# Performance work log

Measured on AMD Instinct MI355X. Metric: run time of the kernel, lower is better.

## Reference

```python
import jax, jax.numpy as jnp
import numpy as np

B, S, H, V, L = 2, 1024, 2048, 32000, 8


def _ternary(w):
    """BitNet-1.58 style per-tensor ternary quantization with STE."""
    scale = jnp.mean(jnp.abs(w))
    wq = jnp.clip(jnp.round(w / (scale + 1e-8)), -1.0, 1.0) * scale
    # straight-through: forward value is wq, gradient flows to w
    return w + jax.lax.stop_gradient(wq - w)


def _layernorm(x, g, b, eps=1e-5):
    m = jnp.mean(x, axis=-1, keepdims=True)
    v = jnp.var(x, axis=-1, keepdims=True)
    return (x - m) / jnp.sqrt(v + eps) * g + b


def setup_inputs() -> dict:
    key = jax.random.key(0)
    ks = jax.random.split(key, 5)
    return {
        "input_ids": jax.random.randint(ks[0], (B, S), 0, V),
        "embed": jax.random.normal(ks[1], (V, H), jnp.float32) * 0.02,
        "layer_w": jax.random.normal(ks[2], (L, H, H), jnp.float32) * 0.02,
        "layer_b": jnp.zeros((L, H), jnp.float32),
        "ln_g": jnp.ones((L, H), jnp.float32),
        "ln_b": jnp.zeros((L, H), jnp.float32),
        "final_g": jnp.ones((H,), jnp.float32),
        "final_b": jnp.zeros((H,), jnp.float32),
        "head_w": jax.random.normal(ks[3], (V, H), jnp.float32) * 0.02,
    }


def reference(input_ids, embed, layer_w, layer_b, ln_g, ln_b, final_g, final_b, head_w):
    # embedding lookup: (B, S, H)
    h = embed[input_ids]

    def step(h, params):
        w, b, g, bb = params
        y = jnp.einsum("bsh,oh->bso", h, _ternary(w)) + b  # ternary linear
        h = _layernorm(y + h, g, bb)                        # residual + LN
        return h, None

    h, _ = jax.lax.scan(step, h, (layer_w, layer_b, ln_g, ln_b))
    h = _layernorm(h, final_g, final_b)
    logits = jnp.einsum("bsh,vh->bsv", h, _ternary(head_w))  # (B, S, V)
    return logits
```

## Files before the change

kernel.cpp:

```cpp
#include <hip/hip_runtime.h>


#define H 2048
#define MTOK 2048
#define VOC 32000
#define NL 8
#define BK 64

typedef __attribute__((ext_vector_type(8))) _Float16 f16x8;
typedef __attribute__((ext_vector_type(4))) float f32x4;

__device__ __forceinline__ unsigned short f2h(float f) {
  _Float16 h = (_Float16)f;
  union { _Float16 h; unsigned short u; } v; v.h = h;
  return v.u;
}

__global__ void abssum_kernel(const float* __restrict__ w, int n, long nstride,
                              float* __restrict__ out) {
  __shared__ float sbuf[4];
  const float* wp = w + (long)blockIdx.y * nstride;
  int tid = blockIdx.x * blockDim.x + threadIdx.x;
  int stride = gridDim.x * blockDim.x * 4;
  float s = 0.f;
  for (int i = tid * 4; i < n; i += stride) {
    float4 v = *reinterpret_cast<const float4*>(wp + i);
    s += fabsf(v.x) + fabsf(v.y) + fabsf(v.z) + fabsf(v.w);
  }
#pragma unroll
  for (int off = 32; off > 0; off >>= 1) s += __shfl_down(s, off);
  if ((threadIdx.x & 63) == 0) sbuf[threadIdx.x >> 6] = s;
  __syncthreads();
  if (threadIdx.x == 0) atomicAdd(out + blockIdx.y, sbuf[0] + sbuf[1] + sbuf[2] + sbuf[3]);
}

__global__ void quantize_kernel(const float* __restrict__ w, int n,
                                const float* __restrict__ sumptr, float cnt,
                                unsigned short* __restrict__ T) {
  float scale = *sumptr / cnt;
  float spe = scale + 1e-8f;
  int tid = blockIdx.x * blockDim.x + threadIdx.x;
  int stride = gridDim.x * blockDim.x * 4;
  for (int i = tid * 4; i < n; i += stride) {
    float4 v = *reinterpret_cast<const float4*>(w + i);
    ushort4 t;
    t.x = f2h(fminf(fmaxf(rintf(v.x / spe), -1.f), 1.f));
    t.y = f2h(fminf(fmaxf(rintf(v.y / spe), -1.f), 1.f));
    t.z = f2h(fminf(fmaxf(rintf(v.z / spe), -1.f), 1.f));
    t.w = f2h(fminf(fmaxf(rintf(v.w / spe), -1.f), 1.f));
    *reinterpret_cast<ushort4*>(T + i) = t;
  }
}

__global__ void gather_split_kernel(const int* __restrict__ ids, const float* __restrict__ embed,
                                    float* __restrict__ h, unsigned short* __restrict__ act) {
  int t = blockIdx.x;
  long src = (long)ids[t] * H;
  long dst = (long)t * H;
  for (int c = threadIdx.x * 4; c < H; c += blockDim.x * 4) {
    float4 v = *reinterpret_cast<const float4*>(embed + src + c);
    *reinterpret_cast<float4*>(h + dst + c) = v;
    ushort4 u;
    u.x = f2h(v.x); u.y = f2h(v.y); u.z = f2h(v.z); u.w = f2h(v.w);
    *reinterpret_cast<ushort4*>(act + dst + c) = u;
  }
}

__device__ __forceinline__ float block_sum(float v, float* sbuf) {
#pragma unroll
  for (int off = 32; off > 0; off >>= 1) v += __shfl_down(v, off);
  int lane = threadIdx.x & 63, w = threadIdx.x >> 6;
  if (lane == 0) sbuf[w] = v;
  __syncthreads();
  float r = sbuf[0] + sbuf[1] + sbuf[2] + sbuf[3];
  __syncthreads();
  return r;
}

__global__ void ln_kernel(const float* __restrict__ x_in, const float* __restrict__ resid,
                          const float* __restrict__ g, const float* __restrict__ b,
                          float* __restrict__ hout, unsigned short* __restrict__ act) {
  __shared__ float sbuf[4];
  int t = blockIdx.x;
  long base = (long)t * H;
  int c0 = threadIdx.x * 8;
  float x[8];
#pragma unroll
  for (int j = 0; j < 8; j += 4) {
    float4 v = *reinterpret_cast<const float4*>(x_in + base + c0 + j);
    x[j] = v.x; x[j + 1] = v.y; x[j + 2] = v.z; x[j + 3] = v.w;
  }
  if (resid != nullptr) {
#pragma unroll
    for (int j = 0; j < 8; j += 4) {
      float4 v = *reinterpret_cast<const float4*>(resid + base + c0 + j);
      x[j] += v.x; x[j + 1] += v.y; x[j + 2] += v.z; x[j + 3] += v.w;
    }
  }
  float s = 0.f;
#pragma unroll
  for (int j = 0; j < 8; ++j) s += x[j];
  s = block_sum(s, sbuf);
  float m = s * (1.f / H);
  float vs = 0.f;
#pragma unroll
  for (int j = 0; j < 8; ++j) { float d = x[j] - m; vs += d * d; }
  vs = block_sum(vs, sbuf);
  float r = 1.f / sqrtf(vs * (1.f / H) + 1e-5f);
  float o[8];
#pragma unroll
  for (int j = 0; j < 8; ++j) o[j] = (x[j] - m) * r * g[c0 + j] + b[c0 + j];
  if (hout != nullptr) {
#pragma unroll
    for (int j = 0; j < 8; j += 4) {
      float4 v; v.x = o[j]; v.y = o[j + 1]; v.z = o[j + 2]; v.w = o[j + 3];
      *reinterpret_cast<float4*>(hout + base + c0 + j) = v;
    }
  }
#pragma unroll
  for (int j = 0; j < 8; j += 4) {
    ushort4 u;
    u.x = f2h(o[j]); u.y = f2h(o[j + 1]); u.z = f2h(o[j + 2]); u.w = f2h(o[j + 3]);
    *reinterpret_cast<ushort4*>(act + base + c0 + j) = u;
  }
}

__device__ __forceinline__ void gll16(const void* g, void* l) {
  __builtin_amdgcn_global_load_lds((const __attribute__((address_space(1))) void*)g,
                                   (__attribute__((address_space(3))) void*)l, 16, 0, 0);
}

template <int ROWS>
__device__ __forceinline__ void stage_tile(unsigned short* sdst, const unsigned short* G,
                                           long row0, int k0, long ldk, int tid) {
  int wv = tid >> 6, lane = tid & 63;
  int c = lane & 7;
  int r8 = lane >> 3;
  int cs = c ^ r8;
#pragma unroll
  for (int i = 0; i < ROWS / 32; ++i) {
    int blk = i * 4 + wv;
    int row = blk * 8 + r8;
    const unsigned short* g = G + (row0 + row) * ldk + (k0 + cs * 8);
    gll16((const void*)g, (void*)(sdst + blk * 512));
  }
}

template <int TBM, int TBN, int WR, int WC, int MF, int NF, bool HAS_BIAS>
__global__ __launch_bounds__(256)
void gemm_t(const unsigned short* __restrict__ A, const unsigned short* __restrict__ Bt,
            const float* __restrict__ bias, const float* __restrict__ sumptr, float cnt,
            float* __restrict__ C, int N, int K, int nrb) {
  __shared__ unsigned short sA[2][TBM * BK];
  __shared__ unsigned short sB[2][TBN * BK];
  int tid = threadIdx.x;
  int lane = tid & 63, wid = tid >> 6;
  int wr = wid / WC, wc = wid % WC;

  int nwg = gridDim.x;
  int bid = blockIdx.x;
  int chunk = nwg >> 3;
  int swz = (bid & 7) * chunk + (bid >> 3);
  int rb = swz % nrb, cbl = swz / nrb;
  long row0 = (long)rb * TBM;
  long col0 = (long)cbl * TBN;

  f32x4 acc[MF][NF] = {};

  int rsel = lane & 15;
  int hi = lane >> 4;
  int lx = lane & 7;

  int NT = K >> 6;
  stage_tile<TBM>(sA[0], A, row0, 0, K, tid);
  stage_tile<TBN>(sB[0], Bt, col0, 0, K, tid);

  for (int t = 0; t < NT; ++t) {
    __syncthreads();
    int nb = (t + 1) & 1;
    if (t + 1 < NT) {
      stage_tile<TBM>(sA[nb], A, row0, (t + 1) << 6, K, tid);
      stage_tile<TBN>(sB[nb], Bt, col0, (t + 1) << 6, K, tid);
    }
    const unsigned short* pA = sA[t & 1];
    const unsigned short* pB = sB[t & 1];
#pragma unroll
    for (int kk = 0; kk < 2; ++kk) {
      int seg = (kk * 4 + hi) ^ lx;
      f16x8 af[MF], bf[NF];
#pragma unroll
      for (int f = 0; f < MF; ++f) {
        int ra = wr * (MF * 16) + f * 16 + rsel;
        af[f] = *reinterpret_cast<const f16x8*>(&pA[ra * BK + seg * 8]);
      }
#pragma unroll
      for (int f = 0; f < NF; ++f) {
        int rn = wc * (NF * 16) + f * 16 + rsel;
        bf[f] = *reinterpret_cast<const f16x8*>(&pB[rn * BK + seg * 8]);
      }
#pragma unroll
      for (int mf = 0; mf < MF; ++mf)
#pragma unroll
        for (int nf = 0; nf < NF; ++nf)
          acc[mf][nf] = __builtin_amdgcn_mfma_f32_16x16x32_f16(af[mf], bf[nf], acc[mf][nf], 0, 0, 0);
    }
  }

  float scale = *sumptr / cnt;
#pragma unroll
  for (int mf = 0; mf < MF; ++mf) {
    long grow0 = row0 + wr * (MF * 16) + mf * 16 + hi * 4;
#pragma unroll
    for (int nf = 0; nf < NF; ++nf) {
      long gcol = col0 + wc * (NF * 16) + nf * 16 + rsel;
      float bv = HAS_BIAS ? bias[gcol] : 0.f;
#pragma unroll
      for (int r = 0; r < 4; ++r) {
        C[(grow0 + r) * (long)N + gcol] = acc[mf][nf][r] * scale + bv;
      }
    }
  }
}

extern "C" void kernel_launch(void* const* d_in, const int* in_sizes, int n_in,
                              void* d_out, int out_size, void* d_ws, size_t ws_size,
                              hipStream_t stream) {
  const int* input_ids = (const int*)d_in[0];
  const float* embed   = (const float*)d_in[1];
  const float* layer_w = (const float*)d_in[2];
  const float* layer_b = (const float*)d_in[3];
  const float* ln_g    = (const float*)d_in[4];
  const float* ln_b    = (const float*)d_in[5];
  const float* final_g = (const float*)d_in[6];
  const float* final_b = (const float*)d_in[7];
  const float* head_w  = (const float*)d_in[8];
  float* out = (float*)d_out;

  char* ws = (char*)d_ws;
  size_t off = 0;
  auto take = [&](size_t bytes) -> void* {
    void* p = ws + off;
    off = (off + bytes + 255) & ~(size_t)255;
    return p;
  };
  float* sums        = (float*)take(16 * sizeof(float));
  unsigned short* Tl = (unsigned short*)take((size_t)H * H * 2);
  unsigned short* Th = (unsigned short*)take((size_t)VOC * H * 2);
  float* hbuf        = (float*)take((size_t)MTOK * H * 4);
  float* ybuf        = (float*)take((size_t)MTOK * H * 4);
  unsigned short* act = (unsigned short*)take((size_t)MTOK * H * 2);
  (void)ws_size; (void)in_sizes; (void)n_in; (void)out_size;

  hipMemsetAsync(sums, 0, 16 * sizeof(float), stream);

  abssum_kernel<<<dim3(512, NL), 256, 0, stream>>>(layer_w, H * H, (long)H * H, sums);
  abssum_kernel<<<dim3(2048, 1), 256, 0, stream>>>(head_w, VOC * H, 0, sums + 8);

  quantize_kernel<<<4096, 256, 0, stream>>>(head_w, VOC * H, sums + 8, (float)((size_t)VOC * H), Th);

  gather_split_kernel<<<MTOK, 256, 0, stream>>>(input_ids, embed, hbuf, act);

  for (int l = 0; l < NL; ++l) {
    quantize_kernel<<<1024, 256, 0, stream>>>(layer_w + (size_t)l * H * H, H * H, sums + l,
                                              (float)(H * H), Tl);
    gemm_t<128, 64, 4, 1, 2, 4, true><<<512, 256, 0, stream>>>(
        act, Tl, layer_b + (size_t)l * H, sums + l, (float)(H * H), ybuf, H, H, MTOK / 128);
    ln_kernel<<<MTOK, 256, 0, stream>>>(ybuf, hbuf, ln_g + (size_t)l * H, ln_b + (size_t)l * H,
                                        hbuf, act);
  }

  ln_kernel<<<MTOK, 256, 0, stream>>>(hbuf, nullptr, final_g, final_b, nullptr, act);

  gemm_t<128, 128, 2, 2, 4, 4, false><<<4000, 256, 0, stream>>>(
      act, Th, nullptr, sums + 8, (float)((size_t)VOC * H), out, VOC, H, MTOK / 128);
}
```

Baseline: 1.478 ms.

## Add 256x256 pipelined head GEMM and batch layer weight quantization

Replaces the head projection GEMM with a new 256x256-tile kernel that uses 512 threads, double-buffered LDS, direct global-to-LDS loads and a four-phase schedule interleaving loads with MFMA, with setprio and barriers. It also quantizes all eight layer weight matrices in one batched launch when workspace allows, instead of once per layer. The intent is higher MFMA utilization and fewer launches on the dominant vocab GEMM, at the cost of a larger LDS footprint, extra workspace and hand-tuned waitcnt logic that could be fragile.

```diff
diff --git a/kernel.cpp b/kernel.cpp
--- a/kernel.cpp
+++ b/kernel.cpp
@@ -34,21 +34,23 @@
   if (threadIdx.x == 0) atomicAdd(out + blockIdx.y, sbuf[0] + sbuf[1] + sbuf[2] + sbuf[3]);
 }
 
-__global__ void quantize_kernel(const float* __restrict__ w, int n,
-                                const float* __restrict__ sumptr, float cnt,
-                                unsigned short* __restrict__ T) {
-  float scale = *sumptr / cnt;
+__global__ void quantize_kernel(const float* __restrict__ w, int n, long nstride,
+                                const float* __restrict__ sums, int sbase, float cnt,
+                                unsigned short* __restrict__ T, long tstride) {
+  float scale = sums[sbase + blockIdx.y] / cnt;
   float spe = scale + 1e-8f;
+  const float* wp = w + (long)blockIdx.y * nstride;
+  unsigned short* tp = T + (long)blockIdx.y * tstride;
   int tid = blockIdx.x * blockDim.x + threadIdx.x;
   int stride = gridDim.x * blockDim.x * 4;
   for (int i = tid * 4; i < n; i += stride) {
-    float4 v = *reinterpret_cast<const float4*>(w + i);
+    float4 v = *reinterpret_cast<const float4*>(wp + i);
     ushort4 t;
     t.x = f2h(fminf(fmaxf(rintf(v.x / spe), -1.f), 1.f));
     t.y = f2h(fminf(fmaxf(rintf(v.y / spe), -1.f), 1.f));
     t.z = f2h(fminf(fmaxf(rintf(v.z / spe), -1.f), 1.f));
     t.w = f2h(fminf(fmaxf(rintf(v.w / spe), -1.f), 1.f));
-    *reinterpret_cast<ushort4*>(T + i) = t;
+    *reinterpret_cast<ushort4*>(tp + i) = t;
   }
 }
 
@@ -217,6 +219,157 @@
 #pragma unroll
       for (int r = 0; r < 4; ++r) {
         C[(grow0 + r) * (long)N + gcol] = acc[mf][nf][r] * scale + bv;
+      }
+    }
+  }
+}
+
+
+__device__ __forceinline__ void stage_unitA(const unsigned short* G, long row0, int k0, long ldk,
+                                            unsigned short* slot, int r, int widx, int lane) {
+  int r8 = lane >> 3, cs = (lane & 7) ^ r8;
+#pragma unroll
+  for (int j = 0; j < 2; ++j) {
+    int trow = j * 128 + r * 64 + widx * 8;
+    const unsigned short* g = G + (row0 + trow + r8) * ldk + (k0 + cs * 8);
+    gll16((const void*)g, (void*)(slot + trow * 64));
+  }
+}
+
+__device__ __forceinline__ void stage_unitB(const unsigned short* G, long col0, int k0, long ldk,
+                                            unsigned short* slot, int c, int widx, int lane) {
+  int r8 = lane >> 3, cs = (lane & 7) ^ r8;
+#pragma unroll
+  for (int j = 0; j < 2; ++j) {
+    int u = j * 8 + widx;
+    int trow = (u >> 2) * 64 + c * 32 + (u & 3) * 8;
+    const unsigned short* g = G + (col0 + trow + r8) * ldk + (k0 + cs * 8);
+    gll16((const void*)g, (void*)(slot + trow * 64));
+  }
+}
+
+template <int R, int C>
+__device__ __forceinline__ void phase_read(const unsigned short* pA, const unsigned short* pB,
+                                           int wr, int wc, int rsel, int hi, int lx,
+                                           f16x8 (&af)[4][2], f16x8 (&bf)[2][2]) {
+#pragma unroll
+  for (int kk = 0; kk < 2; ++kk) {
+    int seg = (kk * 4 + hi) ^ lx;
+#pragma unroll
+    for (int mf = 0; mf < 4; ++mf) {
+      int ra = wr * 128 + R * 64 + mf * 16 + rsel;
+      af[mf][kk] = *reinterpret_cast<const f16x8*>(&pA[ra * 64 + seg * 8]);
+    }
+#pragma unroll
+    for (int nf = 0; nf < 2; ++nf) {
+      int rb = wc * 64 + C * 32 + nf * 16 + rsel;
+      bf[nf][kk] = *reinterpret_cast<const f16x8*>(&pB[rb * 64 + seg * 8]);
+    }
+  }
+}
+
+template <int R, int C>
+__device__ __forceinline__ void phase_mfma(const f16x8 (&af)[4][2], const f16x8 (&bf)[2][2],
+                                           f32x4 (&acc)[8][4]) {
+#pragma unroll
+  for (int kk = 0; kk < 2; ++kk)
+#pragma unroll
+    for (int mf = 0; mf < 4; ++mf)
+#pragma unroll
+      for (int nf = 0; nf < 2; ++nf)
+        acc[R * 4 + mf][C * 2 + nf] = __builtin_amdgcn_mfma_f32_16x16x32_f16(
+            af[mf][kk], bf[nf][kk], acc[R * 4 + mf][C * 2 + nf], 0, 0, 0);
+}
+
+#define PHASE(RR, CC, STAGE_STMT, DO_WAIT4)                                  \
+  {                                                                          \
+    f16x8 af[4][2], bf[2][2];                                                \
+    phase_read<RR, CC>(pA, pB, wr, wc, rsel, hi, lx, af, bf);                \
+    STAGE_STMT;                                                              \
+    if (DO_WAIT4) asm volatile("s_waitcnt vmcnt(4)" ::: "memory");           \
+    asm volatile("s_barrier" ::: "memory");                                  \
+    asm volatile("s_waitcnt lgkmcnt(0)" ::: "memory");                       \
+    __builtin_amdgcn_sched_barrier(0);                                       \
+    __builtin_amdgcn_s_setprio(1);                                           \
+    phase_mfma<RR, CC>(af, bf, acc);                                         \
+    __builtin_amdgcn_s_setprio(0);                                           \
+    asm volatile("s_barrier" ::: "memory");                                  \
+  }
+
+__global__ __launch_bounds__(512, 2)
+void gemm256(const unsigned short* __restrict__ A, const unsigned short* __restrict__ Bt,
+             const float* __restrict__ sumptr, float cnt,
+             float* __restrict__ C, int N, int K, int nrb) {
+  __shared__ unsigned short sA[2][256 * 64];
+  __shared__ unsigned short sB[2][256 * 64];
+  int tid = threadIdx.x, lane = tid & 63, widx = tid >> 6;
+  int wr = widx >> 2, wc = widx & 3;
+  int rsel = lane & 15, hi = lane >> 4, lx = lane & 7;
+
+  int nwg = gridDim.x, bid = blockIdx.x, chunk = nwg >> 3;
+  int swz = (bid & 7) * chunk + (bid >> 3);
+  int rb = swz % nrb, cb = swz / nrb;
+  long row0 = (long)rb * 256, col0 = (long)cb * 256;
+
+  f32x4 acc[8][4] = {};
+
+  int NT = K >> 6;
+  stage_unitA(A, row0, 0, K, sA[0], 0, widx, lane);
+  stage_unitB(Bt, col0, 0, K, sB[0], 0, widx, lane);
+  stage_unitB(Bt, col0, 0, K, sB[0], 1, widx, lane);
+  stage_unitA(A, row0, 0, K, sA[0], 1, widx, lane);
+  asm volatile("s_waitcnt vmcnt(4)" ::: "memory");
+  asm volatile("s_barrier" ::: "memory");
+
+  for (int t = 0; t < NT - 1; ++t) {
+    const unsigned short* pA = sA[t & 1];
+    const unsigned short* pB = sB[t & 1];
+    unsigned short* qA = sA[(t + 1) & 1];
+    unsigned short* qB = sB[(t + 1) & 1];
+    int k1 = (t + 1) << 6;
+    PHASE(0, 0, stage_unitA(A, row0, k1, K, qA, 0, widx, lane), true)
+    PHASE(0, 1, stage_unitB(Bt, col0, k1, K, qB, 0, widx, lane), true)
+    PHASE(1, 1, stage_unitB(Bt, col0, k1, K, qB, 1, widx, lane), false)
+    PHASE(1, 0, stage_unitA(A, row0, k1, K, qA, 1, widx, lane), true)
+  }
+
+  asm volatile("s_waitcnt vmcnt(0)" ::: "memory");
+  asm volatile("s_barrier" ::: "memory");
+  {
+    const unsigned short* pA = sA[(NT - 1) & 1];
+    const unsigned short* pB = sB[(NT - 1) & 1];
+    {
+      f16x8 af[4][2], bf[2][2];
+      phase_read<0, 0>(pA, pB, wr, wc, rsel, hi, lx, af, bf);
+      phase_mfma<0, 0>(af, bf, acc);
+    }
+    {
+      f16x8 af[4][2], bf[2][2];
+      phase_read<0, 1>(pA, pB, wr, wc, rsel, hi, lx, af, bf);
+      phase_mfma<0, 1>(af, bf, acc);
+    }
+    {
+      f16x8 af[4][2], bf[2][2];
+      phase_read<1, 1>(pA, pB, wr, wc, rsel, hi, lx, af, bf);
+      phase_mfma<1, 1>(af, bf, acc);
+    }
+    {
+      f16x8 af[4][2], bf[2][2];
+      phase_read<1, 0>(pA, pB, wr, wc, rsel, hi, lx, af, bf);
+      phase_mfma<1, 0>(af, bf, acc);
+    }
+  }
+
+  float scale = *sumptr / cnt;
+#pragma unroll
+  for (int m = 0; m < 8; ++m) {
+    long grow0 = row0 + wr * 128 + m * 16 + hi * 4;
+#pragma unroll
+    for (int n = 0; n < 4; ++n) {
+      long gcol = col0 + wc * 64 + n * 16 + rsel;
+#pragma unroll
+      for (int r = 0; r < 4; ++r) {
+        C[(grow0 + r) * (long)N + gcol] = acc[m][n][r] * scale;
       }
     }
   }
@@ -243,34 +396,46 @@
     off = (off + bytes + 255) & ~(size_t)255;
     return p;
   };
+  size_t need_batched = (size_t)16 * 4 + (size_t)NL * H * H * 2 + (size_t)VOC * H * 2 +
+                        2 * (size_t)MTOK * H * 4 + (size_t)MTOK * H * 2 + 6 * 256;
+  bool batched = ws_size >= need_batched;
+
   float* sums        = (float*)take(16 * sizeof(float));
-  unsigned short* Tl = (unsigned short*)take((size_t)H * H * 2);
+  unsigned short* Tl = (unsigned short*)take((batched ? (size_t)NL : 1) * H * H * 2);
   unsigned short* Th = (unsigned short*)take((size_t)VOC * H * 2);
   float* hbuf        = (float*)take((size_t)MTOK * H * 4);
   float* ybuf        = (float*)take((size_t)MTOK * H * 4);
   unsigned short* act = (unsigned short*)take((size_t)MTOK * H * 2);
-  (void)ws_size; (void)in_sizes; (void)n_in; (void)out_size;
+  (void)in_sizes; (void)n_in; (void)out_size;
 
   hipMemsetAsync(sums, 0, 16 * sizeof(float), stream);
 
   abssum_kernel<<<dim3(512, NL), 256, 0, stream>>>(layer_w, H * H, (long)H * H, sums);
   abssum_kernel<<<dim3(2048, 1), 256, 0, stream>>>(head_w, VOC * H, 0, sums + 8);
 
-  quantize_kernel<<<4096, 256, 0, stream>>>(head_w, VOC * H, sums + 8, (float)((size_t)VOC * H), Th);
+  quantize_kernel<<<dim3(4096, 1), 256, 0, stream>>>(head_w, VOC * H, 0, sums, 8,
+                                                     (float)((size_t)VOC * H), Th, 0);
+  if (batched) {
+    quantize_kernel<<<dim3(1024, NL), 256, 0, stream>>>(layer_w, H * H, (long)H * H, sums, 0,
+                                                        (float)(H * H), Tl, (long)H * H);
+  }
 
   gather_split_kernel<<<MTOK, 256, 0, stream>>>(input_ids, embed, hbuf, act);
 
   for (int l = 0; l < NL; ++l) {
-    quantize_kernel<<<1024, 256, 0, stream>>>(layer_w + (size_t)l * H * H, H * H, sums + l,
-                                              (float)(H * H), Tl);
+    unsigned short* Tcur = Tl + (batched ? (size_t)l * H * H : 0);
+    if (!batched) {
+      quantize_kernel<<<dim3(1024, 1), 256, 0, stream>>>(layer_w + (size_t)l * H * H, H * H, 0,
+                                                         sums, l, (float)(H * H), Tcur, 0);
+    }
     gemm_t<128, 64, 4, 1, 2, 4, true><<<512, 256, 0, stream>>>(
-        act, Tl, layer_b + (size_t)l * H, sums + l, (float)(H * H), ybuf, H, H, MTOK / 128);
+        act, Tcur, layer_b + (size_t)l * H, sums + l, (float)(H * H), ybuf, H, H, MTOK / 128);
     ln_kernel<<<MTOK, 256, 0, stream>>>(ybuf, hbuf, ln_g + (size_t)l * H, ln_b + (size_t)l * H,
                                         hbuf, act);
   }
 
   ln_kernel<<<MTOK, 256, 0, stream>>>(hbuf, nullptr, final_g, final_b, nullptr, act);
 
-  gemm_t<128, 128, 2, 2, 4, 4, false><<<4000, 256, 0, stream>>>(
-      act, Th, nullptr, sums + 8, (float)((size_t)VOC * H), out, VOC, H, MTOK / 128);
-}
+  gemm256<<<1000, 512, 0, stream>>>(act, Th, sums + 8, (float)((size_t)VOC * H), out, VOC, H,
+                                    MTOK / 256);
+}
```

After: 1.442 ms. 2.4% less time.

## Use vmcnt-based pipelining, larger head GEMM tiles, and batched layer quantization

Applied to the files above, without the earlier changes.

The GEMM main loop replaces __syncthreads with an explicit s_waitcnt vmcnt on the previous tile's async LDS loads plus raw s_barrier, so the next tile's prefetch stays in flight while the current one is consumed. The vocab head GEMM moves to 256x256 tiles with 512 threads (8 waves) for more reuse per block. Layer weight quantization is batched into one launch across all layers when workspace allows, removing per-layer quantize launches. The risks are correctness of the hand-counted vmcnt values, since the barriers drop the compiler's implicit waits, and higher register pressure from the large tile.

```diff
diff --git a/kernel.cpp b/kernel.cpp
--- a/kernel.cpp
+++ b/kernel.cpp
@@ -34,21 +34,23 @@
   if (threadIdx.x == 0) atomicAdd(out + blockIdx.y, sbuf[0] + sbuf[1] + sbuf[2] + sbuf[3]);
 }
 
-__global__ void quantize_kernel(const float* __restrict__ w, int n,
-                                const float* __restrict__ sumptr, float cnt,
-                                unsigned short* __restrict__ T) {
-  float scale = *sumptr / cnt;
+__global__ void quantize_kernel(const float* __restrict__ w, int n, long nstride,
+                                const float* __restrict__ sums, int sbase, float cnt,
+                                unsigned short* __restrict__ T, long tstride) {
+  float scale = sums[sbase + blockIdx.y] / cnt;
   float spe = scale + 1e-8f;
+  const float* wp = w + (long)blockIdx.y * nstride;
+  unsigned short* tp = T + (long)blockIdx.y * tstride;
   int tid = blockIdx.x * blockDim.x + threadIdx.x;
   int stride = gridDim.x * blockDim.x * 4;
   for (int i = tid * 4; i < n; i += stride) {
-    float4 v = *reinterpret_cast<const float4*>(w + i);
+    float4 v = *reinterpret_cast<const float4*>(wp + i);
     ushort4 t;
     t.x = f2h(fminf(fmaxf(rintf(v.x / spe), -1.f), 1.f));
     t.y = f2h(fminf(fmaxf(rintf(v.y / spe), -1.f), 1.f));
     t.z = f2h(fminf(fmaxf(rintf(v.z / spe), -1.f), 1.f));
     t.w = f2h(fminf(fmaxf(rintf(v.w / spe), -1.f), 1.f));
-    *reinterpret_cast<ushort4*>(T + i) = t;
+    *reinterpret_cast<ushort4*>(tp + i) = t;
   }
 }
 
@@ -130,80 +132,80 @@
                                    (__attribute__((address_space(3))) void*)l, 16, 0, 0);
 }
 
-template <int ROWS>
+template <int ROWS, int NTH>
 __device__ __forceinline__ void stage_tile(unsigned short* sdst, const unsigned short* G,
                                            long row0, int k0, long ldk, int tid) {
+  constexpr int WPB = NTH / 64;
   int wv = tid >> 6, lane = tid & 63;
-  int c = lane & 7;
   int r8 = lane >> 3;
-  int cs = c ^ r8;
-#pragma unroll
-  for (int i = 0; i < ROWS / 32; ++i) {
-    int blk = i * 4 + wv;
+  int cs = (lane & 7) ^ r8;
+#pragma unroll
+  for (int i = 0; i < (ROWS / 8) / WPB; ++i) {
+    int blk = i * WPB + wv;
     int row = blk * 8 + r8;
     const unsigned short* g = G + (row0 + row) * ldk + (k0 + cs * 8);
     gll16((const void*)g, (void*)(sdst + blk * 512));
   }
 }
 
-template <int TBM, int TBN, int WR, int WC, int MF, int NF, bool HAS_BIAS>
-__global__ __launch_bounds__(256)
-void gemm_t(const unsigned short* __restrict__ A, const unsigned short* __restrict__ Bt,
-            const float* __restrict__ bias, const float* __restrict__ sumptr, float cnt,
-            float* __restrict__ C, int N, int K, int nrb) {
+template <int TBM, int TBN, int NTH, int WC, int MF, int NF, bool HAS_BIAS>
+__global__ __launch_bounds__(NTH, NTH == 512 ? 2 : 3)
+void gemm_cnt(const unsigned short* __restrict__ A, const unsigned short* __restrict__ Bt,
+              const float* __restrict__ bias, const float* __restrict__ sumptr, float cnt,
+              float* __restrict__ C, int N, int K, int nrb) {
   __shared__ unsigned short sA[2][TBM * BK];
   __shared__ unsigned short sB[2][TBN * BK];
-  int tid = threadIdx.x;
-  int lane = tid & 63, wid = tid >> 6;
+  constexpr int WAITN = (TBM + TBN) / (NTH / 8);
+  static_assert(WAITN == 6 || WAITN == 8, "unsupported wait count");
+
+  int tid = threadIdx.x, lane = tid & 63, wid = tid >> 6;
   int wr = wid / WC, wc = wid % WC;
-
-  int nwg = gridDim.x;
-  int bid = blockIdx.x;
-  int chunk = nwg >> 3;
+  int rsel = lane & 15, hi = lane >> 4, lx = lane & 7;
+
+  int nwg = gridDim.x, bid = blockIdx.x, chunk = nwg >> 3;
   int swz = (bid & 7) * chunk + (bid >> 3);
   int rb = swz % nrb, cbl = swz / nrb;
-  long row0 = (long)rb * TBM;
-  long col0 = (long)cbl * TBN;
+  long row0 = (long)rb * TBM, col0 = (long)cbl * TBN;
 
   f32x4 acc[MF][NF] = {};
-
-  int rsel = lane & 15;
-  int hi = lane >> 4;
-  int lx = lane & 7;
-
   int NT = K >> 6;
-  stage_tile<TBM>(sA[0], A, row0, 0, K, tid);
-  stage_tile<TBN>(sB[0], Bt, col0, 0, K, tid);
+
+  stage_tile<TBM, NTH>(sA[0], A, row0, 0, K, tid);
+  stage_tile<TBN, NTH>(sB[0], Bt, col0, 0, K, tid);
 
   for (int t = 0; t < NT; ++t) {
-    __syncthreads();
-    int nb = (t + 1) & 1;
+    int cur = t & 1;
     if (t + 1 < NT) {
-      stage_tile<TBM>(sA[nb], A, row0, (t + 1) << 6, K, tid);
-      stage_tile<TBN>(sB[nb], Bt, col0, (t + 1) << 6, K, tid);
-    }
-    const unsigned short* pA = sA[t & 1];
-    const unsigned short* pB = sB[t & 1];
+      stage_tile<TBM, NTH>(sA[cur ^ 1], A, row0, (t + 1) << 6, K, tid);
+      stage_tile<TBN, NTH>(sB[cur ^ 1], Bt, col0, (t + 1) << 6, K, tid);
+      if constexpr (WAITN == 8) asm volatile("s_waitcnt vmcnt(8)" ::: "memory");
+      else                      asm volatile("s_waitcnt vmcnt(6)" ::: "memory");
+    } else {
+      asm volatile("s_waitcnt vmcnt(0)" ::: "memory");
+    }
+    asm volatile("s_barrier" ::: "memory");
+
+    const unsigned short* pA = sA[cur];
+    const unsigned short* pB = sB[cur];
 #pragma unroll
     for (int kk = 0; kk < 2; ++kk) {
       int seg = (kk * 4 + hi) ^ lx;
       f16x8 af[MF], bf[NF];
 #pragma unroll
-      for (int f = 0; f < MF; ++f) {
-        int ra = wr * (MF * 16) + f * 16 + rsel;
-        af[f] = *reinterpret_cast<const f16x8*>(&pA[ra * BK + seg * 8]);
-      }
-#pragma unroll
-      for (int f = 0; f < NF; ++f) {
-        int rn = wc * (NF * 16) + f * 16 + rsel;
-        bf[f] = *reinterpret_cast<const f16x8*>(&pB[rn * BK + seg * 8]);
-      }
+      for (int mf = 0; mf < MF; ++mf)
+        af[mf] = *reinterpret_cast<const f16x8*>(
+            &pA[(wr * (MF * 16) + mf * 16 + rsel) * BK + seg * 8]);
+#pragma unroll
+      for (int nf = 0; nf < NF; ++nf)
+        bf[nf] = *reinterpret_cast<const f16x8*>(
+            &pB[(wc * (NF * 16) + nf * 16 + rsel) * BK + seg * 8]);
 #pragma unroll
       for (int mf = 0; mf < MF; ++mf)
 #pragma unroll
         for (int nf = 0; nf < NF; ++nf)
           acc[mf][nf] = __builtin_amdgcn_mfma_f32_16x16x32_f16(af[mf], bf[nf], acc[mf][nf], 0, 0, 0);
     }
+    asm volatile("s_barrier" ::: "memory");
   }
 
   float scale = *sumptr / cnt;
@@ -243,34 +245,46 @@
     off = (off + bytes + 255) & ~(size_t)255;
     return p;
   };
+  size_t need_batched = (size_t)16 * 4 + (size_t)NL * H * H * 2 + (size_t)VOC * H * 2 +
+                        2 * (size_t)MTOK * H * 4 + (size_t)MTOK * H * 2 + 6 * 256;
+  bool batched = ws_size >= need_batched;
+
   float* sums        = (float*)take(16 * sizeof(float));
-  unsigned short* Tl = (unsigned short*)take((size_t)H * H * 2);
+  unsigned short* Tl = (unsigned short*)take((batched ? (size_t)NL : 1) * H * H * 2);
   unsigned short* Th = (unsigned short*)take((size_t)VOC * H * 2);
   float* hbuf        = (float*)take((size_t)MTOK * H * 4);
   float* ybuf        = (float*)take((size_t)MTOK * H * 4);
   unsigned short* act = (unsigned short*)take((size_t)MTOK * H * 2);
-  (void)ws_size; (void)in_sizes; (void)n_in; (void)out_size;
+  (void)in_sizes; (void)n_in; (void)out_size;
 
   hipMemsetAsync(sums, 0, 16 * sizeof(float), stream);
 
   abssum_kernel<<<dim3(512, NL), 256, 0, stream>>>(layer_w, H * H, (long)H * H, sums);
   abssum_kernel<<<dim3(2048, 1), 256, 0, stream>>>(head_w, VOC * H, 0, sums + 8);
 
-  quantize_kernel<<<4096, 256, 0, stream>>>(head_w, VOC * H, sums + 8, (float)((size_t)VOC * H), Th);
+  quantize_kernel<<<dim3(4096, 1), 256, 0, stream>>>(head_w, VOC * H, 0, sums, 8,
+                                                     (float)((size_t)VOC * H), Th, 0);
+  if (batched) {
+    quantize_kernel<<<dim3(1024, NL), 256, 0, stream>>>(layer_w, H * H, (long)H * H, sums, 0,
+                                                        (float)(H * H), Tl, (long)H * H);
+  }
 
   gather_split_kernel<<<MTOK, 256, 0, stream>>>(input_ids, embed, hbuf, act);
 
   for (int l = 0; l < NL; ++l) {
-    quantize_kernel<<<1024, 256, 0, stream>>>(layer_w + (size_t)l * H * H, H * H, sums + l,
-                                              (float)(H * H), Tl);
-    gemm_t<128, 64, 4, 1, 2, 4, true><<<512, 256, 0, stream>>>(
-        act, Tl, layer_b + (size_t)l * H, sums + l, (float)(H * H), ybuf, H, H, MTOK / 128);
+    unsigned short* Tcur = Tl + (batched ? (size_t)l * H * H : 0);
+    if (!batched) {
+      quantize_kernel<<<dim3(1024, 1), 256, 0, stream>>>(layer_w + (size_t)l * H * H, H * H, 0,
+                                                         sums, l, (float)(H * H), Tcur, 0);
+    }
+    gemm_cnt<128, 64, 256, 1, 2, 4, true><<<512, 256, 0, stream>>>(
+        act, Tcur, layer_b + (size_t)l * H, sums + l, (float)(H * H), ybuf, H, H, MTOK / 128);
     ln_kernel<<<MTOK, 256, 0, stream>>>(ybuf, hbuf, ln_g + (size_t)l * H, ln_b + (size_t)l * H,
                                         hbuf, act);
   }
 
   ln_kernel<<<MTOK, 256, 0, stream>>>(hbuf, nullptr, final_g, final_b, nullptr, act);
 
-  gemm_t<128, 128, 2, 2, 4, 4, false><<<4000, 256, 0, stream>>>(
-      act, Th, nullptr, sums + 8, (float)((size_t)VOC * H), out, VOC, H, MTOK / 128);
-}
+  gemm_cnt<256, 256, 512, 4, 8, 4, false><<<1000, 512, 0, stream>>>(
+      act, Th, nullptr, sums + 8, (float)((size_t)VOC * H), out, VOC, H, MTOK / 256);
+}
```

After: 1.382 ms. -6.5%, faster.
